# Optimization experiments

Hardware: AMD Instinct MI355X
Metric: run time of the kernel (lower is better)

Reference implementation:

```python
import jax, jax.numpy as jnp
import numpy as np
import math

A = 32; B = 32; PSIZE = 16; K = 3; STRIDE = 2; PAD = 1; ITERS = 3; FINAL_LAMBDA = 0.01
KK = K * K; KKA = KK * A; KKA2 = KKA // 2 + 1
EPS = 1e-12; LN2PI = math.log(2 * math.pi)


def unfold(x, k, s, p):
    # torch F.unfold: output feature dim ordered (C, kh, kw), columns row-major
    b, C, h, w = x.shape
    xp = jnp.pad(x, ((0, 0), (0, 0), (p, p), (p, p)))
    oh = (h + 2 * p - k) // s + 1
    ow = (w + 2 * p - k) // s + 1
    cols = [xp[:, :, ki:ki + s * (oh - 1) + 1:s, kj:kj + s * (ow - 1) + 1:s]
            for ki in range(k) for kj in range(k)]
    patches = jnp.stack(cols, axis=2)  # [b, C, kk, oh, ow]
    return patches.reshape(b, C, k * k, oh * ow), oh, ow


def setup_inputs():
    key = jax.random.key(0)
    ks = jax.random.split(key, 8)
    b, h, w = 4, 14, 14
    a_in = jax.random.uniform(ks[0], (b, A, h, w), dtype=jnp.float32)
    pose = jax.random.normal(ks[1], (b, A * PSIZE, h, w), dtype=jnp.float32)
    mpose_w = jax.random.normal(ks[2], (B * PSIZE, PSIZE), dtype=jnp.float32) / np.float32(np.sqrt(PSIZE))
    mpose_b = jnp.zeros((B * PSIZE,), jnp.float32)
    freq_w = jax.random.normal(ks[3], (KKA2, PSIZE, 2), dtype=jnp.float32) * 0.02
    ln_g = jnp.ones((A,), jnp.float32)
    ln_b = jnp.zeros((A,), jnp.float32)
    lim = np.float32(np.sqrt(6.0 / (KK + KK)))  # xavier_uniform on [kk, kk, 1]
    spat_w = jax.random.uniform(ks[4], (KK, KK, 1), jnp.float32, -lim, lim)
    spat_bias = jnp.ones((KK,), jnp.float32)
    beta_u = jnp.zeros((1, 1, B, 1), jnp.float32)
    beta_a = jnp.zeros((1, 1, B), jnp.float32)
    return dict(a_in=a_in, pose=pose, mpose_w=mpose_w, mpose_b=mpose_b,
                freq_w=freq_w, ln_g=ln_g, ln_b=ln_b, spat_w=spat_w,
                spat_bias=spat_bias, beta_u=beta_u, beta_a=beta_a)


def _forward(a_in, pose, mpose_w, mpose_b, freq_w, ln_g, ln_b,
             spat_w, spat_bias, beta_u, beta_a):
    b = a_in.shape[0]
    pose_u, oh, ow = unfold(pose, K, STRIDE, PAD)  # [b, A*PSIZE, KK, l]
    l = oh * ow
    pose_u = pose_u.reshape(b, A, PSIZE, KK, l)
    pose_u = pose_u.transpose(0, 4, 3, 1, 2).reshape(b, l, KKA, PSIZE)
    # mpose linear: psize -> B*psize
    po = jnp.einsum('blkp,qp->blkq', pose_u, mpose_w) + mpose_b
    po = po.reshape(b * l, KKA, B, PSIZE)
    # Frequency FFT filter over kkA axis (weight shared across all B slices)
    xf = jnp.fft.rfft(po, axis=1, norm='ortho')        # [bl, KKA2, B, PSIZE] complex
    wc = freq_w[..., 0] + 1j * freq_w[..., 1]           # [KKA2, PSIZE]
    xf = xf * wc[None, :, None, :]
    po = jnp.fft.irfft(xf, n=KKA, axis=1, norm='ortho') + po  # residual
    v = po.reshape(b, l, KKA, B, PSIZE)
    a_u, _, _ = unfold(a_in, K, STRIDE, PAD)            # [b, A, KK, l]
    a_u = a_u.transpose(0, 3, 2, 1).reshape(b, l, KKA)
    # Spatial gating applied to ones-initialized r (identical for every B slice)
    ones = jnp.ones((b * l, KKA), jnp.float32)
    g = ones.reshape(b * l, KK, A)
    mu_g = g.mean(-1, keepdims=True)
    var_g = ((g - mu_g) ** 2).mean(-1, keepdims=True)
    gn = (g - mu_g) / jnp.sqrt(var_g + 1e-5) * ln_g + ln_b
    g2 = jnp.einsum('ij,nja->nia', spat_w[:, :, 0], gn) + spat_bias[None, :, None]
    gate = jax.nn.gelu(g2, approximate=False).reshape(b * l, KKA) + ones
    logit = jnp.broadcast_to(gate[:, :, None], (b * l, KKA, B))
    r = jax.nn.softmax(logit, axis=2).reshape(b, l, KKA, B, 1)
    a_out = mu = None
    for i in range(ITERS):
        lam = FINAL_LAMBDA * (1.0 - 0.95 ** (i + 1))
        # m-step
        rr = r * a_u[:, :, :, None, None]
        r_sum = rr.sum(axis=2, keepdims=True)                 # [b,l,1,B,1]
        coeff = rr / (r_sum + EPS)
        mu = (coeff * v).sum(axis=2, keepdims=True)           # [b,l,1,B,PSIZE]
        sig = (coeff * (v - mu) ** 2).sum(axis=2, keepdims=True) + EPS
        cost = (beta_u + jnp.log(jnp.sqrt(sig[:, :, 0]))) * r_sum[:, :, 0]  # [b,l,B,PSIZE]
        a_out = jax.nn.sigmoid(lam * (beta_a - cost.sum(axis=3)))           # [b,l,B]
        if i < ITERS - 1:
            # e-step (note: log(sigma_sq * ln2pi) is faithful to the original code)
            ln_p = (-0.5 * jnp.sum(jnp.log(sig * LN2PI), axis=-1)
                    - jnp.sum((v - mu) ** 2 / (2.0 * sig), axis=-1))        # [b,l,KKA,B]
            ln_ap = ln_p + jnp.log(a_out[:, :, None, :])
            r = jax.nn.softmax(ln_ap, axis=-1)[..., None]
    pose_out = mu[:, :, 0].reshape(b, l, B * PSIZE).transpose(0, 2, 1).reshape(b, B * PSIZE, oh, ow)
    a_fin = a_out.transpose(0, 2, 1).reshape(b, B, oh, ow)
    return a_fin, pose_out


def reference(a_in, pose, mpose_w, mpose_b, freq_w, ln_g, ln_b,
              spat_w, spat_bias, beta_u, beta_a):
    return _forward(a_in, pose, mpose_w, mpose_b, freq_w, ln_g, ln_b,
                    spat_w, spat_bias, beta_u, beta_a)
```

## Files before the change

kernel.cpp:

```cpp
#include <hip/hip_runtime.h>
#include <hip/hip_bf16.h>
#include <math.h>

#define A_    32
#define B_    32
#define PS    16
#define KK_   9
#define KKA_  288
#define OH_   7
#define L_    49
#define NB    4
#define NSITE 196

#define LAM1 5.0e-4f
#define LAM2 9.75e-4f
#define LAM3 1.42625e-3f
#define LOG_LN2PI 0.6086775903077413f

typedef _Float16 half2v __attribute__((ext_vector_type(2)));
typedef _Float16 half4v __attribute__((ext_vector_type(4)));
typedef short    short8 __attribute__((ext_vector_type(8)));
typedef float    floatx4 __attribute__((ext_vector_type(4)));

#if defined(__has_attribute)
#  if __has_attribute(amdgpu_num_vgpr)
#    define KEM_VGPR_ATTR __attribute__((amdgpu_num_vgpr(224)))
#  else
#    define KEM_VGPR_ATTR
#  endif
#else
#  define KEM_VGPR_ATTR
#endif

static __device__ __forceinline__ float san(float x, float lo, float hi){
    return fminf(fmaxf(x, lo), hi);
}

static __device__ __forceinline__ float dot2acc(half2v a, half2v b, float c){
#if __has_builtin(__builtin_amdgcn_fdot2)
    return __builtin_amdgcn_fdot2(a, b, c, false);
#else
    return c + (float)a.x*(float)b.x + (float)a.y*(float)b.y;
#endif
}

static __device__ __forceinline__ void sched_fence(){
#if __has_builtin(__builtin_amdgcn_sched_barrier)
    __builtin_amdgcn_sched_barrier(0);
#else
    asm volatile("" ::: "memory");
#endif
}

__global__ void k_prep(const float* __restrict__ fw, const float* __restrict__ pose,
                       ushort* __restrict__ cpr, float* __restrict__ csum,
                       __hip_bfloat16* __restrict__ Xt, int n0, int cols, int nc)
{
    if ((int)blockIdx.x < nc){
        int id = (int)blockIdx.x*256 + threadIdx.x;
        if (id >= 16*288) return;
        int p = id / 288, m = id % 288;
        float acc = fw[(0*16 + p)*2 + 0];
        for (int k = 1; k <= 143; ++k){
            float re = fw[(k*16 + p)*2 + 0];
            float im = fw[(k*16 + p)*2 + 1];
            int km = (k*m) % 288;
            float ang = 0.021816615649929116f * (float)km;
            float s, c; __sincosf(ang, &s, &c);
            acc += 2.0f*(re*c - im*s);
        }
        float re144 = fw[(144*16 + p)*2 + 0];
        acc += re144 * ((m & 1) ? -1.0f : 1.0f);
        float cv = acc * (1.0f/288.0f);
        if (m == 0) cv += 1.0f;
        cv = san(cv, -1e4f, 1e4f);

        __hip_bfloat16 hb = __float2bfloat16(cv);
        float hif = __bfloat162float(hb);
        __hip_bfloat16 lb = __float2bfloat16(cv - hif);
        ushort hi = *(ushort*)&hb, lo = *(ushort*)&lb;

        ushort* c0h = cpr + p*592;
        ushort* c1h = cpr + 16*592   + p*592;
        ushort* c0l = cpr + 16*592*2 + p*592;
        ushort* c1l = cpr + 16*592*3 + p*592;
        int x1 = 288 - m;
        c0h[x1] = hi;  c0l[x1] = lo;
        c1h[x1-1] = hi; c1l[x1-1] = lo;
        if (m >= 1){
            int x2 = 576 - m;
            c0h[x2] = hi;  c0l[x2] = lo;
            c1h[x2-1] = hi; c1l[x2-1] = lo;
        } else {
            c0h[0] = hi; c0l[0] = lo;
            csum[p] = san(1.0f + fw[(0*16 + p)*2 + 0], -1e4f, 1e4f);
        }
        return;
    }
    int id = ((int)blockIdx.x - nc)*256 + threadIdx.x;
    if (id >= cols*KKA_) return;
    int c = id / KKA_, j = id % KKA_;
    int n = n0 + (c >> 4), q = c & 15;
    int bs = n / L_, l = n % L_, oy = l / OH_, ox = l % OH_;
    int kk = j >> 5, a = j & 31;
    int y = oy*2 - 1 + kk/3, x = ox*2 - 1 + kk%3;
    float v = 0.f;
    if ((unsigned)y < 14u && (unsigned)x < 14u)
        v = pose[((bs*(A_*PS) + a*PS + q)*14 + y)*14 + x];
    Xt[id] = __float2bfloat16(san(v, -1e4f, 1e4f));
}

__launch_bounds__(256)
__global__ void k_stageB(const ushort* __restrict__ cpr, const __hip_bfloat16* __restrict__ Xt,
                         _Float16* __restrict__ U, int cols, int ns)
{
    const int bx = blockIdx.x, by = blockIdx.y, p = blockIdx.z;
    const int t = threadIdx.x;
    const int w = t >> 6, lane = t & 63;
    const int mn = lane & 15, quad = lane >> 4;
    const int i0 = by*48;
    const int col = bx*64 + w*16 + mn;
    const int colc = (col < cols) ? col : (cols - 1);

    const ushort* c0h = cpr + p*592;
    const ushort* c1h = cpr + 16*592   + p*592;
    const ushort* c0l = cpr + 16*592*2 + p*592;
    const ushort* c1l = cpr + 16*592*3 + p*592;

    floatx4 acc[3] = {{0,0,0,0},{0,0,0,0},{0,0,0,0}};
    for (int k0 = 0; k0 < 288; k0 += 32){
        short8 bfrag = *(const short8*)&Xt[colc*KKA_ + k0 + quad*8];
        #pragma unroll
        for (int s = 0; s < 3; ++s){
            int o = 288 + k0 + quad*8 - (i0 + s*16 + mn);
            int sel = o & 1;
            int off = o - sel;
            const ushort* bh = sel ? c1h : c0h;
            const ushort* bl = sel ? c1l : c0l;
            short8 ah = *(const short8*)&bh[off];
            short8 al = *(const short8*)&bl[off];
            acc[s] = __builtin_amdgcn_mfma_f32_16x16x32_bf16(ah, bfrag, acc[s], 0, 0, 0);
            acc[s] = __builtin_amdgcn_mfma_f32_16x16x32_bf16(al, bfrag, acc[s], 0, 0, 0);
        }
    }
    if (col < cols){
        const int nn = col >> 4, q0 = col & 15;
        #pragma unroll
        for (int s = 0; s < 3; ++s){
            #pragma unroll
            for (int r = 0; r < 4; ++r){
                int i = i0 + s*16 + quad*4 + r;
                U[(i*ns + nn)*256 + p*16 + q0] = (_Float16)acc[s][r];
            }
        }
    }
}

__launch_bounds__(512, 2) KEM_VGPR_ATTR
__global__ void
k_em(const _Float16* __restrict__ U, const float* __restrict__ a_in,
     const float* __restrict__ mpw, const float* __restrict__ mpb,
     const float* __restrict__ csum,
     const float* __restrict__ beta_u, const float* __restrict__ beta_a,
     int n0, int ns, float* __restrict__ out)
{
    const int nl = blockIdx.x;
    const int n  = n0 + nl;
    const int t = threadIdx.x;
    const int Bc = t >> 4, p = t & 15;
    const int bs = n / L_, l = n % L_;

    __shared__ uint  v_lds[72][512];
    __shared__ float d_s[48][33];
    __shared__ float a_s[KKA_];
    __shared__ float cst[32];

    for (int j = t; j < KKA_; j += 512){
        int kk = j >> 5, a = j & 31;
        int oy = l / OH_, ox = l % OH_;
        int y = oy*2 - 1 + kk/3, x = ox*2 - 1 + kk%3;
        float v = 0.f;
        if ((unsigned)y < 14u && (unsigned)x < 14u)
            v = a_in[((bs*A_ + a)*14 + y)*14 + x];
        a_s[j] = san(v, 0.f, 1e4f);
    }
    half2v w_h[8];
    #pragma unroll
    for (int k = 0; k < 8; ++k){
        w_h[k].x = (_Float16)mpw[t*16 + 2*k];
        w_h[k].y = (_Float16)mpw[t*16 + 2*k + 1];
    }
    const float vb = mpb[t] * csum[p];
    const float bu = beta_u[Bc];
    const float ba = beta_a[Bc];
    __syncthreads();

    float S0tot = 0.f;
    for (int j = 0; j < KKA_; ++j) S0tot += a_s[j];

    const _Float16* Up = U + nl*256 + p*16;
    const int istr = ns*256;

    float S1 = 0.f, S2 = 0.f;

    half2v v_h[72];
    #pragma unroll
    for (int g = 0; g < 36; ++g){
        #pragma unroll
        for (int k2 = 0; k2 < 2; ++k2){
            const int pr = g*2 + k2;
            const int i0 = 144 + pr*2;
            union { uint4 u4; half2v h2[4]; } A0, A1, B0, B1;
            A0.u4 = *(const uint4*)&Up[i0*istr];
            A1.u4 = *(const uint4*)&Up[i0*istr + 8];
            B0.u4 = *(const uint4*)&Up[(i0+1)*istr];
            B1.u4 = *(const uint4*)&Up[(i0+1)*istr + 8];
            float v0 = vb, v1 = vb;
            #pragma unroll
            for (int m = 0; m < 4; ++m){
                v0 = dot2acc(A0.h2[m], w_h[m],   v0);
                v0 = dot2acc(A1.h2[m], w_h[4+m], v0);
                v1 = dot2acc(B0.h2[m], w_h[m],   v1);
                v1 = dot2acc(B1.h2[m], w_h[4+m], v1);
            }
            const float a0 = a_s[i0], a1 = a_s[i0+1];
            S1 += a0*v0 + a1*v1;
            S2 += a0*v0*v0 + a1*v1*v1;
            half2v vh; vh.x = (_Float16)v0; vh.y = (_Float16)v1;
            v_h[pr] = vh;
        }
        sched_fence();
    }

    for (int ch = 0; ch < 9; ++ch){
        #pragma unroll
        for (int k = 0; k < 8; ++k){
            const int i0 = ch*16 + 2*k;
            union { uint4 u4; half2v h2[4]; } A0, A1, B0, B1;
            A0.u4 = *(const uint4*)&Up[i0*istr];
            A1.u4 = *(const uint4*)&Up[i0*istr + 8];
            B0.u4 = *(const uint4*)&Up[(i0+1)*istr];
            B1.u4 = *(const uint4*)&Up[(i0+1)*istr + 8];
            float v0 = vb, v1 = vb;
            #pragma unroll
            for (int m = 0; m < 4; ++m){
                v0 = dot2acc(A0.h2[m], w_h[m],   v0);
                v0 = dot2acc(A1.h2[m], w_h[4+m], v0);
                v1 = dot2acc(B0.h2[m], w_h[m],   v1);
                v1 = dot2acc(B1.h2[m], w_h[4+m], v1);
            }
            const float a0 = a_s[i0], a1 = a_s[i0+1];
            S1 += a0*v0 + a1*v1;
            S2 += a0*v0*v0 + a1*v1*v1;
            union { half2v h; uint u; } cv;
            cv.h.x = (_Float16)v0; cv.h.y = (_Float16)v1;
            v_lds[ch*8 + k][t] = cv.u;
        }
    }

    float mu_r, i2s_r;
    {
        const float rs  = S0tot * (1.0f/32.0f);
        const float inv = 1.0f / (rs + 1e-12f);
        const float S1r = S1 * (1.0f/32.0f), S2r = S2 * (1.0f/32.0f);
        mu_r = S1r * inv;
        const float sg  = fmaxf((S2r - 2.f*mu_r*S1r + mu_r*mu_r*rs) * inv, 0.f) + 1e-12f;
        i2s_r = 0.5f / sg;
        const float lg  = logf(sg);
        float cs = (bu + 0.5f*lg) * rs;
        float ls = lg + LOG_LN2PI;
        #pragma unroll
        for (int m = 1; m < 16; m <<= 1){ cs += __shfl_xor(cs, m, 16); ls += __shfl_xor(ls, m, 16); }
        const float aout = san(1.f/(1.f + expf(-LAM1*(ba - cs))), 1e-30f, 1.f);
        if (p == 0) cst[Bc] = logf(aout) - 0.5f*ls;
    }
    __syncthreads();

    const int b0 = p & 1, b1 = (p>>1)&1, b2 = (p>>2)&1, b3 = (p>>3)&1;
    float muF = 0.f, aF = 0.f;
    for (int it = 0; it < 2; ++it){
        const float lam = it ? LAM3 : LAM2;
        float T0 = 0.f, T1 = 0.f, T2 = 0.f;

        #pragma unroll
        for (int ch = 0; ch < 6; ++ch){
            #pragma unroll
            for (int g = 0; g < 3; ++g){
                float e1[8], e2[4], e3[2], dfin;
                #pragma unroll
                for (int s = 0; s < 8; ++s){
                    const int pr = ch*24 + g*8 + s;
                    float v0, v1;
                    if (ch < 3){
                        union { uint u; half2v h; } cv; cv.u = v_lds[pr][t];
                        v0 = (float)cv.h.x; v1 = (float)cv.h.y;
                    } else {
                        half2v vh = v_h[pr - 72];
                        v0 = (float)vh.x; v1 = (float)vh.y;
                    }
                    float d0 = v0 - mu_r, d1 = v1 - mu_r;
                    float ea = d0*d0*i2s_r, eb = d1*d1*i2s_r;
                    float aown  = b0 ? eb : ea;
                    float asend = b0 ? ea : eb;
                    e1[s] = aown + __shfl_xor(asend, 1);
                }
                #pragma unroll
                for (int s = 0; s < 4; ++s){
                    float aown  = b1 ? e1[2*s+1] : e1[2*s];
                    float asend = b1 ? e1[2*s]   : e1[2*s+1];
                    e2[s] = aown + __shfl_xor(asend, 2);
                }
                #pragma unroll
                for (int s = 0; s < 2; ++s){
                    float aown  = b2 ? e2[2*s+1] : e2[2*s];
                    float asend = b2 ? e2[2*s]   : e2[2*s+1];
                    e3[s] = aown + __shfl_xor(asend, 4);
                }
                {
                    float aown  = b3 ? e3[1] : e3[0];
                    float asend = b3 ? e3[0] : e3[1];
                    dfin = aown + __shfl_xor(asend, 8);
                }
                d_s[g*16 + p][Bc] = dfin;
            }
            __syncthreads();
            {
                const int isub = t >> 5, Bce = t & 31;
                #pragma unroll
                for (int rr = 0; rr < 3; ++rr){
                    const int row = rr*16 + isub;
                    float lnap = cst[Bce] - d_s[row][Bce];
                    float mx = lnap;
                    #pragma unroll
                    for (int m = 16; m >= 1; m >>= 1) mx = fmaxf(mx, __shfl_xor(mx, m));
                    float ex = expf(lnap - mx);
                    float sm = ex;
                    #pragma unroll
                    for (int m = 16; m >= 1; m >>= 1) sm += __shfl_xor(sm, m);
                    d_s[row][Bce] = (ex / sm) * a_s[ch*48 + row];
                }
            }
            __syncthreads();
            #pragma unroll
            for (int s = 0; s < 24; ++s){
                const int pr = ch*24 + s;
                float v0, v1;
                if (ch < 3){
                    union { uint u; half2v h; } cv; cv.u = v_lds[pr][t];
                    v0 = (float)cv.h.x; v1 = (float)cv.h.y;
                } else {
                    half2v vh = v_h[pr - 72];
                    v0 = (float)vh.x; v1 = (float)vh.y;
                }
                float r0 = d_s[2*s][Bc], r1 = d_s[2*s+1][Bc];
                T0 += r0 + r1;
                T1 += r0*v0 + r1*v1;
                T2 += r0*v0*v0 + r1*v1*v1;
            }
        }
        const float inv = 1.f/(T0 + 1e-12f);
        const float mu  = T1 * inv;
        const float sg  = fmaxf((T2 - 2.f*mu*T1 + mu*mu*T0) * inv, 0.f) + 1e-12f;
        const float lg  = logf(sg);
        float cs = (bu + 0.5f*lg) * T0;
        float ls = lg + LOG_LN2PI;
        #pragma unroll
        for (int m = 1; m < 16; m <<= 1){ cs += __shfl_xor(cs, m, 16); ls += __shfl_xor(ls, m, 16); }
        const float aout = san(1.f/(1.f + expf(-lam*(ba - cs))), 1e-30f, 1.f);
        if (it == 0){
            mu_r = mu; i2s_r = 0.5f/sg;
            if (p == 0) cst[Bc] = logf(aout) - 0.5f*ls;
            __syncthreads();
        } else { muF = mu; aF = aout; }
    }

    if (p == 0) out[bs*(B_*L_) + Bc*L_ + l] = san(aF, 0.f, 1.f);
    out[6272 + (bs*512 + t)*L_ + l] = san(muF, -1e4f, 1e4f);
}

extern "C" void kernel_launch(void* const* d_in, const int* in_sizes, int n_in,
                              void* d_out, int out_size, void* d_ws, size_t ws_size,
                              hipStream_t stream)
{
    const float* a_in   = (const float*)d_in[0];
    const float* pose   = (const float*)d_in[1];
    const float* mpw    = (const float*)d_in[2];
    const float* mpb    = (const float*)d_in[3];
    const float* fw     = (const float*)d_in[4];
    const float* beta_u = (const float*)d_in[9];
    const float* beta_a = (const float*)d_in[10];
    float* out = (float*)d_out;

    char* base = (char*)d_ws;
    float*  csum = (float*)(base + 0);
    ushort* cpr  = (ushort*)(base + 256);

    const int opts[] = {196, 98, 49, 28, 14, 7, 4, 2, 1};
    int ns = 1;
    for (int oi = 0; oi < 9; ++oi){
        size_t need = 76288u + (size_t)156672u * (size_t)opts[oi];
        if (need <= ws_size){ ns = opts[oi]; break; }
    }
    const int G = NSITE / ns;
    const int cols = ns * PS;
    __hip_bfloat16* Xt = (__hip_bfloat16*)(base + 76288);
    _Float16*       Ug = (_Float16*)(base + 76288 + (size_t)9216*ns);

    for (int g = 0; g < G; ++g){
        const int n0 = g * ns;
        const int nx = (cols*KKA_ + 255)/256;
        const int nc = (g == 0) ? 18 : 0;
        k_prep  <<<nx + nc, 256, 0, stream>>>(fw, pose, cpr, csum, Xt, n0, cols, nc);
        k_stageB<<<dim3((cols + 63)/64, 6, 16), 256, 0, stream>>>(cpr, Xt, Ug, cols, ns);
        k_em    <<<ns, 512, 0, stream>>>(Ug, a_in, mpw, mpb, csum, beta_u, beta_a, n0, ns, out);
    }
}
```

Before: 258.2 us.

## Recompute half of votes per EM chunk instead of holding them in registers

```diff
diff --git a/kernel.cpp b/kernel.cpp
--- a/kernel.cpp
+++ b/kernel.cpp
@@ -18,19 +18,8 @@
 #define LOG_LN2PI 0.6086775903077413f
 
 typedef _Float16 half2v __attribute__((ext_vector_type(2)));
-typedef _Float16 half4v __attribute__((ext_vector_type(4)));
 typedef short    short8 __attribute__((ext_vector_type(8)));
 typedef float    floatx4 __attribute__((ext_vector_type(4)));
-
-#if defined(__has_attribute)
-#  if __has_attribute(amdgpu_num_vgpr)
-#    define KEM_VGPR_ATTR __attribute__((amdgpu_num_vgpr(224)))
-#  else
-#    define KEM_VGPR_ATTR
-#  endif
-#else
-#  define KEM_VGPR_ATTR
-#endif
 
 static __device__ __forceinline__ float san(float x, float lo, float hi){
     return fminf(fmaxf(x, lo), hi);
@@ -128,6 +117,7 @@
     const ushort* c1l = cpr + 16*592*3 + p*592;
 
     floatx4 acc[3] = {{0,0,0,0},{0,0,0,0},{0,0,0,0}};
+    #pragma unroll
     for (int k0 = 0; k0 < 288; k0 += 32){
         short8 bfrag = *(const short8*)&Xt[colc*KKA_ + k0 + quad*8];
         #pragma unroll
@@ -156,7 +146,7 @@
     }
 }
 
-__launch_bounds__(512, 2) KEM_VGPR_ATTR
+__launch_bounds__(512, 1)
 __global__ void
 k_em(const _Float16* __restrict__ U, const float* __restrict__ a_in,
      const float* __restrict__ mpw, const float* __restrict__ mpb,
@@ -203,13 +193,11 @@
 
     float S1 = 0.f, S2 = 0.f;
 
-    half2v v_h[72];
     #pragma unroll
-    for (int g = 0; g < 36; ++g){
-        #pragma unroll
-        for (int k2 = 0; k2 < 2; ++k2){
-            const int pr = g*2 + k2;
-            const int i0 = 144 + pr*2;
+    for (int g = 0; g < 18; ++g){
+        #pragma unroll
+        for (int k2 = 0; k2 < 4; ++k2){
+            const int i0 = 144 + (g*4 + k2)*2;
             union { uint4 u4; half2v h2[4]; } A0, A1, B0, B1;
             A0.u4 = *(const uint4*)&Up[i0*istr];
             A1.u4 = *(const uint4*)&Up[i0*istr + 8];
@@ -226,8 +214,6 @@
             const float a0 = a_s[i0], a1 = a_s[i0+1];
             S1 += a0*v0 + a1*v1;
             S2 += a0*v0*v0 + a1*v1*v1;
-            half2v vh; vh.x = (_Float16)v0; vh.y = (_Float16)v1;
-            v_h[pr] = vh;
         }
         sched_fence();
     }
@@ -284,20 +270,46 @@
 
         #pragma unroll
         for (int ch = 0; ch < 6; ++ch){
+            half2v vcache[24];
+            if (ch >= 3){
+                #pragma unroll
+                for (int gs = 0; gs < 12; ++gs){
+                    #pragma unroll
+                    for (int k2 = 0; k2 < 2; ++k2){
+                        const int s = gs*2 + k2;
+                        const int i0 = (ch*24 + s)*2;
+                        union { uint4 u4; half2v h2[4]; } A0, A1, B0, B1;
+                        A0.u4 = *(const uint4*)&Up[i0*istr];
+                        A1.u4 = *(const uint4*)&Up[i0*istr + 8];
+                        B0.u4 = *(const uint4*)&Up[(i0+1)*istr];
+                        B1.u4 = *(const uint4*)&Up[(i0+1)*istr + 8];
+                        float v0 = vb, v1 = vb;
+                        #pragma unroll
+                        for (int m = 0; m < 4; ++m){
+                            v0 = dot2acc(A0.h2[m], w_h[m],   v0);
+                            v0 = dot2acc(A1.h2[m], w_h[4+m], v0);
+                            v1 = dot2acc(B0.h2[m], w_h[m],   v1);
+                            v1 = dot2acc(B1.h2[m], w_h[4+m], v1);
+                        }
+                        half2v vh; vh.x = (_Float16)v0; vh.y = (_Float16)v1;
+                        vcache[s] = vh;
+                    }
+                    sched_fence();
+                }
+            } else {
+                #pragma unroll
+                for (int s = 0; s < 24; ++s){
+                    union { uint u; half2v h; } cv; cv.u = v_lds[ch*24 + s][t];
+                    vcache[s] = cv.h;
+                }
+            }
             #pragma unroll
             for (int g = 0; g < 3; ++g){
                 float e1[8], e2[4], e3[2], dfin;
                 #pragma unroll
                 for (int s = 0; s < 8; ++s){
-                    const int pr = ch*24 + g*8 + s;
-                    float v0, v1;
-                    if (ch < 3){
-                        union { uint u; half2v h; } cv; cv.u = v_lds[pr][t];
-                        v0 = (float)cv.h.x; v1 = (float)cv.h.y;
-                    } else {
-                        half2v vh = v_h[pr - 72];
-                        v0 = (float)vh.x; v1 = (float)vh.y;
-                    }
+                    half2v vh = vcache[g*8 + s];
+                    float v0 = (float)vh.x, v1 = (float)vh.y;
                     float d0 = v0 - mu_r, d1 = v1 - mu_r;
                     float ea = d0*d0*i2s_r, eb = d1*d1*i2s_r;
                     float aown  = b0 ? eb : ea;
@@ -343,15 +355,8 @@
             __syncthreads();
             #pragma unroll
             for (int s = 0; s < 24; ++s){
-                const int pr = ch*24 + s;
-                float v0, v1;
-                if (ch < 3){
-                    union { uint u; half2v h; } cv; cv.u = v_lds[pr][t];
-                    v0 = (float)cv.h.x; v1 = (float)cv.h.y;
-                } else {
-                    half2v vh = v_h[pr - 72];
-                    v0 = (float)vh.x; v1 = (float)vh.y;
-                }
+                half2v vh = vcache[s];
+                float v0 = (float)vh.x, v1 = (float)vh.y;
                 float r0 = d_s[2*s][Bc], r1 = d_s[2*s+1][Bc];
                 T0 += r0 + r1;
                 T1 += r0*v0 + r1*v1;
```

Result: slower. 303.7 us (+17.6%).
